# Performance work log

Hardware: AMD Instinct MI355X
Metric: run time of the kernel (lower is better)

## Reference

```python
import jax, jax.numpy as jnp
import numpy as np

B, T, C, H = 2, 2048, 2048, 16
HD = C // H  # head_dim = 128


def setup_inputs() -> dict:
    key = jax.random.key(0)
    k1, k2, k3 = jax.random.split(key, 3)
    x = jax.random.normal(k1, (B, T, C), dtype=jnp.float32)
    # causal mask: positions with mask==0 are blocked (masked_fill(mask==0, -inf))
    mask = jnp.tril(jnp.ones((T, T), dtype=bool))[None, None]  # [1,1,T,T]
    W_qkv = jax.random.normal(k2, (C, 3 * C), dtype=jnp.float32) * (C ** -0.5)
    W_proj = jax.random.normal(k3, (C, C), dtype=jnp.float32) * (C ** -0.5)
    b_proj = jnp.zeros((C,), dtype=jnp.float32)
    return {"x": x, "mask": mask, "W_qkv": W_qkv, "W_proj": W_proj, "b_proj": b_proj}


def reference(x, mask, W_qkv, W_proj, b_proj):
    # QKV projection (Linear, bias=False)
    qkv = jnp.einsum('btc,cd->btd', x, W_qkv)            # [B,T,3C]
    qkv = qkv.reshape(B, T, 3, H, HD)
    q = qkv[:, :, 0].transpose(0, 2, 1, 3)               # [B,H,T,HD]
    k = qkv[:, :, 1].transpose(0, 2, 1, 3)
    v = qkv[:, :, 2].transpose(0, 2, 1, 3)
    # scaled dot-product attention (dropout is identity in eval)
    att = jnp.einsum('bhqd,bhkd->bhqk', q, k) / jnp.sqrt(jnp.float32(HD))
    att = jnp.where(mask, att, -jnp.inf)
    att = jax.nn.softmax(att, axis=-1)
    y = jnp.einsum('bhqk,bhkd->bhqd', att, v)            # [B,H,T,HD]
    y = y.transpose(0, 2, 1, 3).reshape(B, T, C)
    return jnp.einsum('btc,cd->btd', y, W_proj) + b_proj
```

## Files before the change

### kernel.cpp

```cpp
#include <hip/hip_runtime.h>
#include <hip/hip_bf16.h>

#define B_  2
#define T_  2048
#define C_  2048
#define H_  16
#define HD_ 128

using bf16x8 = __attribute__((ext_vector_type(8))) __bf16;
using f32x4  = __attribute__((ext_vector_type(4))) float;

__device__ __forceinline__ unsigned short f2bs(float f) {
    __hip_bfloat16 h = __float2bfloat16(f);
    return __builtin_bit_cast(unsigned short, h);
}

__device__ __forceinline__ void gload_lds16(const unsigned short* g, unsigned short* l) {
    __builtin_amdgcn_global_load_lds(
        (const __attribute__((address_space(1))) unsigned int*)g,
        (__attribute__((address_space(3))) unsigned int*)l, 16, 0, 0);
}

__global__ void k_f2b(const float* __restrict__ in, unsigned short* __restrict__ out, int n4) {
    int i = blockIdx.x * blockDim.x + threadIdx.x;
    if (i < n4) {
        float4 v = reinterpret_cast<const float4*>(in)[i];
        ushort4 o;
        o.x = f2bs(v.x); o.y = f2bs(v.y); o.z = f2bs(v.z); o.w = f2bs(v.w);
        reinterpret_cast<ushort4*>(out)[i] = o;
    }
}

__global__ __launch_bounds__(256) void k_transpose_f2b(const float* __restrict__ in,
                                                       unsigned short* __restrict__ out,
                                                       int K, int N) {
    __shared__ unsigned short t[64][65];
    int k0 = blockIdx.y * 64, n0 = blockIdx.x * 64;
    int tid = threadIdx.x;
#pragma unroll
    for (int p = 0; p < 4; ++p) {
        int idx = p * 256 + tid;
        int r = idx >> 4, c = (idx & 15) << 2;
        float4 v = *reinterpret_cast<const float4*>(in + (long)(k0 + r) * N + n0 + c);
        t[r][c] = f2bs(v.x); t[r][c + 1] = f2bs(v.y);
        t[r][c + 2] = f2bs(v.z); t[r][c + 3] = f2bs(v.w);
    }
    __syncthreads();
#pragma unroll
    for (int p = 0; p < 4; ++p) {
        int idx = p * 256 + tid;
        int r = idx >> 4, c = (idx & 15) << 2;
        ushort4 o;
        o.x = t[c][r]; o.y = t[c + 1][r]; o.z = t[c + 2][r]; o.w = t[c + 3][r];
        *reinterpret_cast<ushort4*>(out + (long)(n0 + r) * K + k0 + c) = o;
    }
}

template <int MODE>
__global__ __launch_bounds__(256, 2) void k_gemm(const unsigned short* __restrict__ A,
                                                 const unsigned short* __restrict__ Bt,
                                                 int M, int N, int K,
                                                 unsigned short* __restrict__ qkv,
                                                 float* __restrict__ out,
                                                 const float* __restrict__ bias) {
    __shared__ __align__(16) unsigned short lA[128 * 32];
    __shared__ __align__(16) unsigned short lB[128 * 32];

    int tid = threadIdx.x;
    int wave = tid >> 6, lane = tid & 63;
    int quad = lane >> 4, l16 = lane & 15;
    int wr = (wave >> 1) * 64, wc = (wave & 1) * 64;
    int m0 = blockIdx.y * 128, n0 = blockIdx.x * 128;

    int lrow = lane >> 2;
    int lcol = (lane & 3) << 3;
    const unsigned short* gA0 = A + (long)(m0 + wave * 32 + lrow) * K + lcol;
    const unsigned short* gA1 = A + (long)(m0 + wave * 32 + 16 + lrow) * K + lcol;
    const unsigned short* gB0 = Bt + (long)(n0 + wave * 32 + lrow) * K + lcol;
    const unsigned short* gB1 = Bt + (long)(n0 + wave * 32 + 16 + lrow) * K + lcol;
    unsigned short* lA0 = &lA[wave * 1024];
    unsigned short* lA1 = &lA[wave * 1024 + 512];
    unsigned short* lB0 = &lB[wave * 1024];
    unsigned short* lB1 = &lB[wave * 1024 + 512];

    f32x4 zero = {0.f, 0.f, 0.f, 0.f};
    f32x4 acc[4][4];
#pragma unroll
    for (int i = 0; i < 4; ++i)
#pragma unroll
        for (int j = 0; j < 4; ++j) acc[i][j] = zero;

    for (int k0 = 0; k0 < K; k0 += 32) {
        __syncthreads();
        gload_lds16(gA0 + k0, lA0);
        gload_lds16(gA1 + k0, lA1);
        gload_lds16(gB0 + k0, lB0);
        gload_lds16(gB1 + k0, lB1);
        __syncthreads();
        bf16x8 af[4], bfr[4];
#pragma unroll
        for (int i = 0; i < 4; ++i)
            af[i] = *reinterpret_cast<const bf16x8*>(&lA[(wr + i * 16 + l16) * 32 + quad * 8]);
#pragma unroll
        for (int j = 0; j < 4; ++j)
            bfr[j] = *reinterpret_cast<const bf16x8*>(&lB[(wc + j * 16 + l16) * 32 + quad * 8]);
#pragma unroll
        for (int i = 0; i < 4; ++i)
#pragma unroll
            for (int j = 0; j < 4; ++j)
                acc[i][j] = __builtin_amdgcn_mfma_f32_16x16x32_bf16(af[i], bfr[j], acc[i][j], 0, 0, 0);
    }

#pragma unroll
    for (int i = 0; i < 4; ++i) {
#pragma unroll
        for (int j = 0; j < 4; ++j) {
#pragma unroll
            for (int r = 0; r < 4; ++r) {
                int m = m0 + wr + i * 16 + quad * 4 + r;
                int n = n0 + wc + j * 16 + l16;
                float v = acc[i][j][r];
                if (MODE == 0) {
                    int s = n >> 11, col = n & 2047;
                    int h = col >> 7, hd = col & 127;
                    int b = m >> 11, t = m & 2047;
                    long base = (long)s * (B_ * H_ * T_ * HD_);
                    if (s == 2)
                        qkv[base + ((long)(b * H_ + h) * HD_ + hd) * T_ + t] = f2bs(v);
                    else
                        qkv[base + ((long)(b * H_ + h) * T_ + t) * HD_ + hd] = f2bs(v);
                } else {
                    out[(long)m * N + n] = v + bias[n];
                }
            }
        }
    }
}

__global__ __launch_bounds__(256, 3) void k_attn(const unsigned short* __restrict__ qkv,
                                                 unsigned short* __restrict__ y) {
    __shared__ __align__(16) unsigned short lK[64 * 136];
    __shared__ __align__(16) unsigned short lVt[128 * 72];
    __shared__ __align__(16) unsigned short lP[4][16 * 72];

    int tid = threadIdx.x;
    int wave = tid >> 6, lane = tid & 63;
    int quad = lane >> 4, l16 = lane & 15;
    int bh = blockIdx.x;
    int qb = ((int)gridDim.y - 1 - (int)blockIdx.y) * 64;

    const unsigned short* Qh = qkv + (long)bh * (T_ * HD_);
    const unsigned short* Kh = qkv + (long)(B_ * H_) * T_ * HD_ + (long)bh * (T_ * HD_);
    const unsigned short* Vt = qkv + 2L * (B_ * H_) * T_ * HD_ + (long)bh * (HD_ * T_);

    bf16x8 aQ[4];
    int qrow = qb + wave * 16 + l16;
#pragma unroll
    for (int kk = 0; kk < 4; ++kk)
        aQ[kk] = *reinterpret_cast<const bf16x8*>(Qh + (long)qrow * HD_ + kk * 32 + quad * 8);

    float m_s[4], l_s[4];
    f32x4 O[8];
    f32x4 zero = {0.f, 0.f, 0.f, 0.f};
#pragma unroll
    for (int r = 0; r < 4; ++r) { m_s[r] = -1e30f; l_s[r] = 0.f; }
#pragma unroll
    for (int h = 0; h < 8; ++h) O[h] = zero;

    int qmax = qb + wave * 16 + 15;
    const float scl = 0.08838834764831845f;

    for (int kb = 0; kb < qb + 64; kb += 64) {
        __syncthreads();
#pragma unroll
        for (int p = 0; p < 4; ++p) {
            int id = p * 256 + tid;
            int r = id >> 4, cc = (id & 15) << 3;
            *reinterpret_cast<int4*>(&lK[r * 136 + cc]) =
                *reinterpret_cast<const int4*>(Kh + (long)(kb + r) * HD_ + cc);
        }
#pragma unroll
        for (int p = 0; p < 4; ++p) {
            int id = p * 256 + tid;
            int r = id >> 3, cc = (id & 7) << 3;
            *reinterpret_cast<int4*>(&lVt[r * 72 + cc]) =
                *reinterpret_cast<const int4*>(Vt + (long)r * T_ + kb + cc);
        }
        __syncthreads();
        if (kb > qmax) continue;

        f32x4 s[4];
#pragma unroll
        for (int st = 0; st < 4; ++st) s[st] = zero;
#pragma unroll
        for (int kk = 0; kk < 4; ++kk) {
#pragma unroll
            for (int st = 0; st < 4; ++st) {
                bf16x8 b = *reinterpret_cast<const bf16x8*>(
                    &lK[(st * 16 + l16) * 136 + kk * 32 + quad * 8]);
                s[st] = __builtin_amdgcn_mfma_f32_16x16x32_bf16(aQ[kk], b, s[st], 0, 0, 0);
            }
        }

        int qg = qb + wave * 16 + quad * 4;
#pragma unroll
        for (int r = 0; r < 4; ++r) {
            int q = qg + r;
            float x[4];
#pragma unroll
            for (int st = 0; st < 4; ++st)
                x[st] = (kb + st * 16 + l16 <= q) ? s[st][r] * scl : -1e30f;
            float mx = fmaxf(fmaxf(x[0], x[1]), fmaxf(x[2], x[3]));
#pragma unroll
            for (int off = 1; off < 16; off <<= 1) mx = fmaxf(mx, __shfl_xor(mx, off));
            float mn = fmaxf(m_s[r], mx);
            float al = __expf(m_s[r] - mn);
            float p[4], rs = 0.f;
#pragma unroll
            for (int st = 0; st < 4; ++st) { p[st] = __expf(x[st] - mn); rs += p[st]; }
#pragma unroll
            for (int off = 1; off < 16; off <<= 1) rs += __shfl_xor(rs, off);
            m_s[r] = mn;
            l_s[r] = l_s[r] * al + rs;
            int row = quad * 4 + r;
#pragma unroll
            for (int st = 0; st < 4; ++st)
                lP[wave][row * 72 + st * 16 + l16] = f2bs(p[st]);
#pragma unroll
            for (int h = 0; h < 8; ++h) O[h][r] *= al;
        }

#pragma unroll
        for (int kc = 0; kc < 2; ++kc) {
            bf16x8 pf = *reinterpret_cast<const bf16x8*>(
                &lP[wave][l16 * 72 + kc * 32 + quad * 8]);
#pragma unroll
            for (int h = 0; h < 8; ++h) {
                bf16x8 vf = *reinterpret_cast<const bf16x8*>(
                    &lVt[(h * 16 + l16) * 72 + kc * 32 + quad * 8]);
                O[h] = __builtin_amdgcn_mfma_f32_16x16x32_bf16(pf, vf, O[h], 0, 0, 0);
            }
        }
    }

    int b = bh >> 4, hh = bh & 15;
#pragma unroll
    for (int r = 0; r < 4; ++r) {
        int t = qb + wave * 16 + quad * 4 + r;
        float inv = 1.f / l_s[r];
#pragma unroll
        for (int h = 0; h < 8; ++h)
            y[(long)(b * T_ + t) * C_ + hh * HD_ + h * 16 + l16] = f2bs(O[h][r] * inv);
    }
}

extern "C" void kernel_launch(void* const* d_in, const int* in_sizes, int n_in,
                              void* d_out, int out_size, void* d_ws, size_t ws_size,
                              hipStream_t stream) {
    const float* x     = (const float*)d_in[0];
    const float* Wqkv  = (const float*)d_in[2];
    const float* Wproj = (const float*)d_in[3];
    const float* bproj = (const float*)d_in[4];
    float* out = (float*)d_out;

    unsigned short* XB     = (unsigned short*)d_ws;
    unsigned short* WQKVT  = XB + 8388608;
    unsigned short* WPROJT = WQKVT + 12582912;
    unsigned short* QKV    = WPROJT + 4194304;
    if (ws_size < 100663296) return;

    k_f2b<<<8192, 256, 0, stream>>>(x, XB, 8388608 / 4);
    k_transpose_f2b<<<dim3(6144 / 64, 2048 / 64), 256, 0, stream>>>(Wqkv, WQKVT, 2048, 6144);
    k_transpose_f2b<<<dim3(2048 / 64, 2048 / 64), 256, 0, stream>>>(Wproj, WPROJT, 2048, 2048);
    k_gemm<0><<<dim3(6144 / 128, 4096 / 128), 256, 0, stream>>>(XB, WQKVT, 4096, 6144, 2048,
                                                                QKV, nullptr, nullptr);
    k_attn<<<dim3(32, 32), 256, 0, stream>>>(QKV, XB);
    k_gemm<1><<<dim3(2048 / 128, 4096 / 128), 256, 0, stream>>>(XB, WPROJT, 4096, 2048, 2048,
                                                                nullptr, out, bproj);
}
```

Baseline: 431.4 us.

## Merge prep kernels into one launch and double K-step per GEMM barrier

```diff
diff --git a/kernel.cpp b/kernel.cpp
--- a/kernel.cpp
+++ b/kernel.cpp
@@ -21,22 +21,34 @@
         (__attribute__((address_space(3))) unsigned int*)l, 16, 0, 0);
 }
 
-__global__ void k_f2b(const float* __restrict__ in, unsigned short* __restrict__ out, int n4) {
-    int i = blockIdx.x * blockDim.x + threadIdx.x;
-    if (i < n4) {
-        float4 v = reinterpret_cast<const float4*>(in)[i];
+__global__ __launch_bounds__(256) void k_prep(const float* __restrict__ x,
+                                              unsigned short* __restrict__ XB,
+                                              const float* __restrict__ Wqkv,
+                                              unsigned short* __restrict__ WQKVT,
+                                              const float* __restrict__ Wproj,
+                                              unsigned short* __restrict__ WPROJT) {
+    __shared__ unsigned short t[64][65];
+    int blk = blockIdx.x;
+    int tid = threadIdx.x;
+    if (blk < 8192) {
+        int i = blk * 256 + tid;
+        float4 v = reinterpret_cast<const float4*>(x)[i];
         ushort4 o;
         o.x = f2bs(v.x); o.y = f2bs(v.y); o.z = f2bs(v.z); o.w = f2bs(v.w);
-        reinterpret_cast<ushort4*>(out)[i] = o;
-    }
-}
-
-__global__ __launch_bounds__(256) void k_transpose_f2b(const float* __restrict__ in,
-                                                       unsigned short* __restrict__ out,
-                                                       int K, int N) {
-    __shared__ unsigned short t[64][65];
-    int k0 = blockIdx.y * 64, n0 = blockIdx.x * 64;
-    int tid = threadIdx.x;
+        reinterpret_cast<ushort4*>(XB)[i] = o;
+        return;
+    }
+    const float* in;
+    unsigned short* out;
+    int K = 2048, N, bx, by;
+    if (blk < 11264) {
+        in = Wqkv; out = WQKVT; N = 6144;
+        bx = (blk - 8192) % 96; by = (blk - 8192) / 96;
+    } else {
+        in = Wproj; out = WPROJT; N = 2048;
+        bx = (blk - 11264) % 32; by = (blk - 11264) / 32;
+    }
+    int k0 = by * 64, n0 = bx * 64;
 #pragma unroll
     for (int p = 0; p < 4; ++p) {
         int idx = p * 256 + tid;
@@ -63,8 +75,8 @@
                                                  unsigned short* __restrict__ qkv,
                                                  float* __restrict__ out,
                                                  const float* __restrict__ bias) {
-    __shared__ __align__(16) unsigned short lA[128 * 32];
-    __shared__ __align__(16) unsigned short lB[128 * 32];
+    __shared__ __align__(16) unsigned short lA[2][128 * 32];
+    __shared__ __align__(16) unsigned short lB[2][128 * 32];
 
     int tid = threadIdx.x;
     int wave = tid >> 6, lane = tid & 63;
@@ -78,10 +90,7 @@
     const unsigned short* gA1 = A + (long)(m0 + wave * 32 + 16 + lrow) * K + lcol;
     const unsigned short* gB0 = Bt + (long)(n0 + wave * 32 + lrow) * K + lcol;
     const unsigned short* gB1 = Bt + (long)(n0 + wave * 32 + 16 + lrow) * K + lcol;
-    unsigned short* lA0 = &lA[wave * 1024];
-    unsigned short* lA1 = &lA[wave * 1024 + 512];
-    unsigned short* lB0 = &lB[wave * 1024];
-    unsigned short* lB1 = &lB[wave * 1024 + 512];
+    int lofs0 = wave * 1024, lofs1 = wave * 1024 + 512;
 
     f32x4 zero = {0.f, 0.f, 0.f, 0.f};
     f32x4 acc[4][4];
@@ -90,25 +99,32 @@
 #pragma unroll
         for (int j = 0; j < 4; ++j) acc[i][j] = zero;
 
-    for (int k0 = 0; k0 < K; k0 += 32) {
-        __syncthreads();
-        gload_lds16(gA0 + k0, lA0);
-        gload_lds16(gA1 + k0, lA1);
-        gload_lds16(gB0 + k0, lB0);
-        gload_lds16(gB1 + k0, lB1);
-        __syncthreads();
-        bf16x8 af[4], bfr[4];
-#pragma unroll
-        for (int i = 0; i < 4; ++i)
-            af[i] = *reinterpret_cast<const bf16x8*>(&lA[(wr + i * 16 + l16) * 32 + quad * 8]);
-#pragma unroll
-        for (int j = 0; j < 4; ++j)
-            bfr[j] = *reinterpret_cast<const bf16x8*>(&lB[(wc + j * 16 + l16) * 32 + quad * 8]);
-#pragma unroll
-        for (int i = 0; i < 4; ++i)
+    for (int k0 = 0; k0 < K; k0 += 64) {
+        __syncthreads();
+#pragma unroll
+        for (int h = 0; h < 2; ++h) {
+            int kk = k0 + h * 32;
+            gload_lds16(gA0 + kk, &lA[h][lofs0]);
+            gload_lds16(gA1 + kk, &lA[h][lofs1]);
+            gload_lds16(gB0 + kk, &lB[h][lofs0]);
+            gload_lds16(gB1 + kk, &lB[h][lofs1]);
+        }
+        __syncthreads();
+#pragma unroll
+        for (int h = 0; h < 2; ++h) {
+            bf16x8 af[4], bfr[4];
+#pragma unroll
+            for (int i = 0; i < 4; ++i)
+                af[i] = *reinterpret_cast<const bf16x8*>(&lA[h][(wr + i * 16 + l16) * 32 + quad * 8]);
 #pragma unroll
             for (int j = 0; j < 4; ++j)
-                acc[i][j] = __builtin_amdgcn_mfma_f32_16x16x32_bf16(af[i], bfr[j], acc[i][j], 0, 0, 0);
+                bfr[j] = *reinterpret_cast<const bf16x8*>(&lB[h][(wc + j * 16 + l16) * 32 + quad * 8]);
+#pragma unroll
+            for (int i = 0; i < 4; ++i)
+#pragma unroll
+                for (int j = 0; j < 4; ++j)
+                    acc[i][j] = __builtin_amdgcn_mfma_f32_16x16x32_bf16(af[i], bfr[j], acc[i][j], 0, 0, 0);
+        }
     }
 
 #pragma unroll
@@ -269,9 +285,7 @@
     unsigned short* QKV    = WPROJT + 4194304;
     if (ws_size < 100663296) return;
 
-    k_f2b<<<8192, 256, 0, stream>>>(x, XB, 8388608 / 4);
-    k_transpose_f2b<<<dim3(6144 / 64, 2048 / 64), 256, 0, stream>>>(Wqkv, WQKVT, 2048, 6144);
-    k_transpose_f2b<<<dim3(2048 / 64, 2048 / 64), 256, 0, stream>>>(Wproj, WPROJT, 2048, 2048);
+    k_prep<<<12288, 256, 0, stream>>>(x, XB, Wqkv, WQKVT, Wproj, WPROJT);
     k_gemm<0><<<dim3(6144 / 128, 4096 / 128), 256, 0, stream>>>(XB, WQKVT, 4096, 6144, 2048,
                                                                 QKV, nullptr, nullptr);
     k_attn<<<dim3(32, 32), 256, 0, stream>>>(QKV, XB);
```

Result: faster. 404.9 us (-6.1%).
